# Performance work log

Hardware: AMD Instinct MI355X
Metric: run time of the kernel (lower is better)

The kernel has to match this reference:

```python
import jax, jax.numpy as jnp
import numpy as np

SHAPES = [(76, 76), (38, 38), (19, 19), (1, 20)]  # 3 feature levels + task-token pseudo-level
D, HEADS, NLVL, NPTS = 256, 8, 4, 4
DH = D // HEADS
NLAYERS = 6
B = 2
S = sum(h * w for h, w in SHAPES)  # 7601


def _ref_points():
    # valid_ratios == 1 (no padding) -> normalized pixel-center grid per level, concatenated. [S,2] (x,y)
    refs = []
    for H, W in SHAPES:
        ry, rx = jnp.meshgrid(jnp.linspace(0.5, H - 0.5, H) / H,
                              jnp.linspace(0.5, W - 0.5, W) / W, indexing='ij')
        refs.append(jnp.stack([rx.ravel(), ry.ravel()], -1))
    return jnp.concatenate(refs, 0)


def _layer_norm(x, g, b):
    m = x.mean(-1, keepdims=True)
    v = ((x - m) ** 2).mean(-1, keepdims=True)
    return (x - m) * jax.lax.rsqrt(v + 1e-5) * g + b


def _bilinear(val_l, locx, locy, H, W):
    # val_l: [B, H*W, HEADS, DH]; locx/locy: [B,Q,HEADS,P] normalized coords.
    # grid_sample semantics: align_corners=False, zero padding.
    v = val_l.transpose(0, 2, 1, 3)  # [B,Hh,HW,DH]
    x = locx * W - 0.5
    y = locy * H - 0.5
    x0 = jnp.floor(x)
    y0 = jnp.floor(y)
    wx1 = x - x0
    wy1 = y - y0

    def corner(xi, yi, w):
        valid = ((xi >= 0) & (xi <= W - 1) & (yi >= 0) & (yi <= H - 1)).astype(v.dtype)
        idx = (jnp.clip(yi, 0, H - 1) * W + jnp.clip(xi, 0, W - 1)).astype(jnp.int32)
        idx_t = idx.transpose(0, 2, 1, 3)  # [B,Hh,Q,P]
        Bq, Hh, Q, P = idx_t.shape
        g = jnp.take_along_axis(v, idx_t.reshape(Bq, Hh, Q * P)[..., None], axis=2)
        g = g.reshape(Bq, Hh, Q, P, DH)
        return g * (w * valid).transpose(0, 2, 1, 3)[..., None]

    return (corner(x0, y0, (1 - wx1) * (1 - wy1)) + corner(x0 + 1, y0, wx1 * (1 - wy1))
            + corner(x0, y0 + 1, (1 - wx1) * wy1) + corner(x0 + 1, y0 + 1, wx1 * wy1))


def _msdeform(q, x, ref, Woff, boff, Wa, ba, Wv, bv, Wo, bo):
    Bq, Sq, _ = x.shape
    value = (x @ Wv + bv).reshape(Bq, Sq, HEADS, DH)
    off = (q @ Woff + boff).reshape(Bq, Sq, HEADS, NLVL, NPTS, 2)
    attn = jax.nn.softmax((q @ Wa + ba).reshape(Bq, Sq, HEADS, NLVL * NPTS), -1)
    attn = attn.reshape(Bq, Sq, HEADS, NLVL, NPTS)
    acc = jnp.zeros((Bq, HEADS, Sq, DH), x.dtype)
    start = 0
    for l, (H, W) in enumerate(SHAPES):
        n = H * W
        loc = ref[None, :, None, None, :] + off[:, :, :, l] / jnp.asarray([W, H], x.dtype)
        samp = _bilinear(value[:, start:start + n], loc[..., 0], loc[..., 1], H, W)  # [B,Hh,S,P,DH]
        a = attn[:, :, :, l].transpose(0, 2, 1, 3)  # [B,Hh,S,P]
        acc = acc + (samp * a[..., None]).sum(3)
        start += n
    return acc.transpose(0, 2, 1, 3).reshape(Bq, Sq, D) @ Wo + bo


def reference(src0, src1, src2, pos0, pos1, pos2, task_encoding, task_pos_enc, level_embed,
              W_off, b_off, W_attn, b_attn, W_val, b_val, W_out, b_out,
              W1, b1, W2, b2, g1, beta1, g2, beta2):
    srcs, poss = [src0, src1, src2], [pos0, pos1, pos2]
    sf, pf = [], []
    for l in range(3):
        Bq, C, H, W = srcs[l].shape
        sf.append(srcs[l].reshape(Bq, C, H * W).transpose(0, 2, 1))
        pf.append(poss[l].reshape(Bq, C, H * W).transpose(0, 2, 1) + level_embed[l])
    sf.append(task_encoding)
    pf.append(jnp.broadcast_to(task_pos_enc[None], task_encoding.shape))
    x = jnp.concatenate(sf, 1)   # [B,S,D]
    pos = jnp.concatenate(pf, 1)
    ref = _ref_points()
    for i in range(NLAYERS):
        q = x + pos
        x = _layer_norm(x + _msdeform(q, x, ref, W_off[i], b_off[i], W_attn[i], b_attn[i],
                                      W_val[i], b_val[i], W_out[i], b_out[i]), g1[i], beta1[i])
        x = _layer_norm(x + jax.nn.relu(x @ W1[i] + b1[i]) @ W2[i] + b2[i], g2[i], beta2[i])
    return x


def setup_inputs() -> dict:
    key = jax.random.key(0)
    ks = jax.random.split(key, 20)
    d = {}
    for i, (H, W) in enumerate(SHAPES[:3]):
        d[f'src{i}'] = jax.random.normal(ks[i], (B, D, H, W), jnp.float32)
        d[f'pos{i}'] = jax.random.normal(ks[3 + i], (B, D, H, W), jnp.float32) * 0.1
    d['task_encoding'] = jax.random.normal(ks[6], (B, 20, D), jnp.float32)
    d['task_pos_enc'] = jax.random.normal(ks[7], (20, D), jnp.float32) * 0.1
    d['level_embed'] = jax.random.normal(ks[8], (NLVL, D), jnp.float32) * 0.1

    def w(k, shape, s=0.02):
        return jax.random.normal(k, shape, jnp.float32) * s

    d['W_off'] = w(ks[9], (NLAYERS, D, HEADS * NLVL * NPTS * 2), 0.01)
    d['b_off'] = w(ks[10], (NLAYERS, HEADS * NLVL * NPTS * 2), 0.2)
    d['W_attn'] = w(ks[11], (NLAYERS, D, HEADS * NLVL * NPTS))
    d['b_attn'] = jnp.zeros((NLAYERS, HEADS * NLVL * NPTS), jnp.float32)
    d['W_val'] = w(ks[12], (NLAYERS, D, D))
    d['b_val'] = jnp.zeros((NLAYERS, D), jnp.float32)
    d['W_out'] = w(ks[13], (NLAYERS, D, D))
    d['b_out'] = jnp.zeros((NLAYERS, D), jnp.float32)
    d['W1'] = w(ks[14], (NLAYERS, D, 2048))
    d['b1'] = jnp.zeros((NLAYERS, 2048), jnp.float32)
    d['W2'] = w(ks[15], (NLAYERS, 2048, D))
    d['b2'] = jnp.zeros((NLAYERS, D), jnp.float32)
    d['g1'] = jnp.ones((NLAYERS, D), jnp.float32)
    d['beta1'] = jnp.zeros((NLAYERS, D), jnp.float32)
    d['g2'] = jnp.ones((NLAYERS, D), jnp.float32)
    d['beta2'] = jnp.zeros((NLAYERS, D), jnp.float32)
    return d
```

## Files before the change

kernel.cpp:

```cpp
#include <hip/hip_runtime.h>

#define S_TOT 7601
#define BATCH 2
#define BM (BATCH * S_TOT)
#define DMODEL 256

typedef unsigned short bf16;
typedef __attribute__((ext_vector_type(8))) short v8s;
typedef __attribute__((ext_vector_type(4))) float v4f;

__device__ __forceinline__ float b2f(bf16 u) {
    union { unsigned int i; float f; } v;
    v.i = ((unsigned int)u) << 16;
    return v.f;
}
__device__ __forceinline__ bf16 f2b(float f) {
    union { unsigned int i; float f; } v;
    v.f = f;
    unsigned int r = v.i + 0x7FFFu + ((v.i >> 16) & 1u);
    return (bf16)(r >> 16);
}
__device__ __forceinline__ float ldin(const void* p, size_t i, int isf32) {
    return isf32 ? ((const float*)p)[i] : b2f(((const bf16*)p)[i]);
}

#define GLDS16(gp, lp)                                                          \
    __builtin_amdgcn_global_load_lds(                                           \
        (const __attribute__((address_space(1))) unsigned int*)(gp),            \
        (__attribute__((address_space(3))) unsigned int*)(lp), 16, 0, 0)

__device__ __forceinline__ void xcd_remap(int& bx, int& by) {
    int gx = gridDim.x, gy = gridDim.y;
    int nwg = gx * gy;
    int lin = blockIdx.y * gx + blockIdx.x;
    int q = nwg >> 3, r = nwg & 7;
    int xcd = lin & 7, idx = lin >> 3;
    int lin2 = (xcd < r ? xcd * (q + 1) : r * (q + 1) + (xcd - r) * q) + idx;
    bx = lin2 % gx;
    by = lin2 / gx;
}

__global__ void detect_dtype(const unsigned short* __restrict__ src, int* __restrict__ flag) {
    __shared__ int cnt;
    if (threadIdx.x == 0) cnt = 0;
    __syncthreads();
    int local = 0;
    for (int i = threadIdx.x; i < 16384; i += 256) {
        unsigned int e = (src[i] >> 7) & 0xFFu;
        if (e >= 143u) local++;
    }
    atomicAdd(&cnt, local);
    __syncthreads();
    if (threadIdx.x == 0) *flag = (cnt > 200) ? 1 : 0;
}

__global__ void __launch_bounds__(256) pack_level(const void* __restrict__ src,
                                                  const void* __restrict__ pin,
                                                  const void* __restrict__ lemb, int lrow,
                                                  float* __restrict__ x,
                                                  bf16* __restrict__ pout,
                                                  int HW, int start,
                                                  const int* __restrict__ flag) {
    int isf32 = *flag;
    int i = blockIdx.x * 256 + threadIdx.x;
    int total = BATCH * HW * 256;
    if (i >= total) return;
    int c = i & 255;
    int t = i >> 8;
    int s = t % HW;
    int b = t / HW;
    size_t src_idx = ((size_t)b * 256 + c) * HW + s;
    float sv = ldin(src, src_idx, isf32);
    float pv = ldin(pin, src_idx, isf32) + ldin(lemb, (size_t)lrow * 256 + c, isf32);
    size_t o = ((size_t)b * S_TOT + start + s) * 256 + c;
    x[o] = sv;
    pout[o] = f2b(pv);
}

__global__ void __launch_bounds__(256) pack_task(const void* __restrict__ te,
                                                 const void* __restrict__ tpe,
                                                 float* __restrict__ x,
                                                 bf16* __restrict__ pout,
                                                 const int* __restrict__ flag) {
    int isf32 = *flag;
    int i = blockIdx.x * 256 + threadIdx.x;
    int total = BATCH * 20 * 256;
    if (i >= total) return;
    int c = i & 255;
    int t = (i >> 8) % 20;
    int b = (i >> 8) / 20;
    size_t o = ((size_t)b * S_TOT + 7581 + t) * 256 + c;
    x[o] = ldin(te, ((size_t)b * 20 + t) * 256 + c, isf32);
    pout[o] = f2b(ldin(tpe, (size_t)t * 256 + c, isf32));
}

__global__ void __launch_bounds__(256) make_ref(float* __restrict__ ref) {
    int s = blockIdx.x * 256 + threadIdx.x;
    if (s >= S_TOT) return;
    int H, W, st;
    if (s < 5776)      { H = 76; W = 76; st = 0; }
    else if (s < 7220) { H = 38; W = 38; st = 5776; }
    else if (s < 7581) { H = 19; W = 19; st = 7220; }
    else               { H = 1;  W = 20; st = 7581; }
    int r = s - st;
    int i = r / W, j = r % W;
    ref[s * 2 + 0] = (j + 0.5f) / (float)W;
    ref[s * 2 + 1] = (i + 0.5f) / (float)H;
}

__global__ void __launch_bounds__(256) cast_out(const float* __restrict__ x,
                                                void* __restrict__ o, int n,
                                                const int* __restrict__ flag) {
    int isf32 = *flag;
    int i = blockIdx.x * 256 + threadIdx.x;
    if (i >= n) return;
    if (isf32) ((float*)o)[i] = x[i];
    else       ((bf16*)o)[i] = f2b(x[i]);
}

__global__ void __launch_bounds__(256) cvt_xq(const float* __restrict__ x,
                                              const bf16* __restrict__ pos,
                                              bf16* __restrict__ xb,
                                              bf16* __restrict__ qb, int n4) {
    int i = blockIdx.x * 256 + threadIdx.x;
    if (i >= n4) return;
    float4 xv = ((const float4*)x)[i];
    ushort4 pv = ((const ushort4*)pos)[i];
    ushort4 xo, qo;
    xo.x = f2b(xv.x); xo.y = f2b(xv.y); xo.z = f2b(xv.z); xo.w = f2b(xv.w);
    qo.x = f2b(xv.x + b2f(pv.x));
    qo.y = f2b(xv.y + b2f(pv.y));
    qo.z = f2b(xv.z + b2f(pv.z));
    qo.w = f2b(xv.w + b2f(pv.w));
    ((ushort4*)xb)[i] = xo;
    ((ushort4*)qb)[i] = qo;
}

__global__ void __launch_bounds__(256) transpose_all(const void* __restrict__ Wv,
                                                     const void* __restrict__ Woff,
                                                     const void* __restrict__ Wa,
                                                     const void* __restrict__ Wo,
                                                     const void* __restrict__ W1,
                                                     const void* __restrict__ W2,
                                                     bf16* __restrict__ Wvt,
                                                     bf16* __restrict__ Wqt,
                                                     bf16* __restrict__ Wot,
                                                     bf16* __restrict__ W1t,
                                                     bf16* __restrict__ W2t,
                                                     int L0, const int* __restrict__ flag) {
    int isf32 = *flag;
    int L = (L0 >= 0) ? L0 : (int)blockIdx.y;
    size_t dl = (L0 >= 0) ? 0 : (size_t)blockIdx.y;
    int t = blockIdx.x;
    const void* src; bf16* dst; int K, N; size_t woff; int rowoff = 0;
    if (t < 64)        { src = Wv;   dst = Wvt + dl * 65536;  K = 256;  N = 256;  woff = (size_t)L * 65536; }
    else if (t < 128)  { src = Woff; dst = Wqt + dl * 98304;  K = 256;  N = 256;  woff = (size_t)L * 65536;  t -= 64; }
    else if (t < 160)  { src = Wa;   dst = Wqt + dl * 98304;  K = 256;  N = 128;  woff = (size_t)L * 32768;  rowoff = 256; t -= 128; }
    else if (t < 224)  { src = Wo;   dst = Wot + dl * 65536;  K = 256;  N = 256;  woff = (size_t)L * 65536;  t -= 160; }
    else if (t < 736)  { src = W1;   dst = W1t + dl * 524288; K = 256;  N = 2048; woff = (size_t)L * 524288; t -= 224; }
    else               { src = W2;   dst = W2t + dl * 524288; K = 2048; N = 256;  woff = (size_t)L * 524288; t -= 736; }
    int ntx = N >> 5;
    int tk = (t / ntx) * 32;
    int tn = (t % ntx) * 32;
    __shared__ float tl[32][33];
    int r = threadIdx.x >> 3;
    int c4 = (threadIdx.x & 7) * 4;
#pragma unroll
    for (int i = 0; i < 4; ++i)
        tl[r][c4 + i] = ldin(src, woff + (size_t)(tk + r) * N + tn + c4 + i, isf32);
    __syncthreads();
#pragma unroll
    for (int i = 0; i < 4; ++i)
        dst[(size_t)(tn + r + rowoff) * K + tk + c4 + i] = f2b(tl[c4 + i][r]);
}

__global__ void __launch_bounds__(256) mfma_gemm(const bf16* __restrict__ A,
                                                 const bf16* __restrict__ Wt,
                                                 const void* __restrict__ bias, size_t boff,
                                                 bf16* __restrict__ C,
                                                 int M, int N, int K, int relu,
                                                 const int* __restrict__ flag) {
    int isf32 = *flag;
    __shared__ __align__(16) char smem[32768];
    bf16* As = (bf16*)smem;
    bf16* Bs = (bf16*)smem + 8192;
    int tid = threadIdx.x;
    int lane = tid & 63, wave = tid >> 6;
    int wm = (wave & 1) << 6, wn = (wave >> 1) << 6;
    int bx, by;
    xcd_remap(bx, by);
    int bm = by * 128, bn = bx * 128;
    int q = lane >> 4, l15 = lane & 15;

    v4f acc[4][4];
#pragma unroll
    for (int i = 0; i < 4; ++i)
#pragma unroll
        for (int j = 0; j < 4; ++j) acc[i][j] = (v4f){0.f, 0.f, 0.f, 0.f};

    int r0 = tid >> 2, r1 = r0 + 64;
    int oct = (tid & 3) * 8;
    int am0 = bm + r0; if (am0 >= M) am0 = M - 1;
    int am1 = bm + r1; if (am1 >= M) am1 = M - 1;
    const bf16* ag0 = A + (size_t)am0 * K + oct;
    const bf16* ag1 = A + (size_t)am1 * K + oct;
    const bf16* bg0 = Wt + (size_t)(bn + r0) * K + oct;
    const bf16* bg1 = Wt + (size_t)(bn + r1) * K + oct;
    bf16* lA0 = As + tid * 8;
    bf16* lA1 = As + (tid + 256) * 8;
    bf16* lA2 = As + 4096 + tid * 8;
    bf16* lA3 = As + 4096 + (tid + 256) * 8;
    bf16* lB0 = Bs + tid * 8;
    bf16* lB1 = Bs + (tid + 256) * 8;
    bf16* lB2 = Bs + 4096 + tid * 8;
    bf16* lB3 = Bs + 4096 + (tid + 256) * 8;

    for (int k0 = 0; k0 < K; k0 += 64) {
        GLDS16(ag0 + k0, lA0);
        GLDS16(ag1 + k0, lA1);
        GLDS16(ag0 + k0 + 32, lA2);
        GLDS16(ag1 + k0 + 32, lA3);
        GLDS16(bg0 + k0, lB0);
        GLDS16(bg1 + k0, lB1);
        GLDS16(bg0 + k0 + 32, lB2);
        GLDS16(bg1 + k0 + 32, lB3);
        __syncthreads();
#pragma unroll
        for (int h = 0; h < 2; ++h) {
            v8s a_frag[4], b_frag[4];
#pragma unroll
            for (int mi = 0; mi < 4; ++mi)
                a_frag[mi] = *(const v8s*)&As[h * 4096 + (wm + mi * 16 + l15) * 32 + q * 8];
#pragma unroll
            for (int ni = 0; ni < 4; ++ni)
                b_frag[ni] = *(const v8s*)&Bs[h * 4096 + (wn + ni * 16 + l15) * 32 + q * 8];
#pragma unroll
            for (int mi = 0; mi < 4; ++mi)
#pragma unroll
                for (int ni = 0; ni < 4; ++ni)
                    acc[mi][ni] = __builtin_amdgcn_mfma_f32_16x16x32_bf16(
                        a_frag[mi], b_frag[ni], acc[mi][ni], 0, 0, 0);
        }
        __syncthreads();
    }

    float bcol[4];
#pragma unroll
    for (int ni = 0; ni < 4; ++ni)
        bcol[ni] = ldin(bias, boff + bn + wn + ni * 16 + l15, isf32);
#pragma unroll
    for (int mi = 0; mi < 4; ++mi) {
        int growb = bm + wm + mi * 16 + q * 4;
#pragma unroll
        for (int r = 0; r < 4; ++r) {
            int gm = growb + r;
            if (gm < M) {
                bf16* rowp = C + (size_t)gm * N + bn + wn + l15;
#pragma unroll
                for (int ni = 0; ni < 4; ++ni) {
                    float v = acc[mi][ni][r] + bcol[ni];
                    if (relu) v = fmaxf(v, 0.f);
                    rowp[ni * 16] = f2b(v);
                }
            }
        }
    }
}

__global__ void __launch_bounds__(256) mfma_gemm64(const bf16* __restrict__ A,
                                                   const bf16* __restrict__ Wt,
                                                   const void* __restrict__ bias, size_t boff,
                                                   bf16* __restrict__ C,
                                                   int M, int N, int K, int relu,
                                                   const int* __restrict__ flag) {
    int isf32 = *flag;
    __shared__ __align__(16) char smem[16384];
    bf16* As = (bf16*)smem;
    bf16* Bs = (bf16*)smem + 4096;
    bf16* Cs = (bf16*)smem;
    int tid = threadIdx.x;
    int lane = tid & 63, wave = tid >> 6;
    int wm = (wave & 1) * 32, wn = (wave >> 1) * 32;
    int bx, by;
    xcd_remap(bx, by);
    int bm = by * 64, bn = bx * 64;
    int q = lane >> 4, l15 = lane & 15;

    v4f acc[2][2];
#pragma unroll
    for (int i = 0; i < 2; ++i)
#pragma unroll
        for (int j = 0; j < 2; ++j) acc[i][j] = (v4f){0.f, 0.f, 0.f, 0.f};

    int srow = tid >> 2;
    int oct = (tid & 3) * 8;
    int am = bm + srow; if (am >= M) am = M - 1;
    const bf16* arow = A + (size_t)am * K + oct;
    const bf16* brow = Wt + (size_t)(bn + srow) * K + oct;
    bf16* lA0 = As + tid * 8;
    bf16* lA1 = As + 2048 + tid * 8;
    bf16* lB0 = Bs + tid * 8;
    bf16* lB1 = Bs + 2048 + tid * 8;

    for (int k0 = 0; k0 < K; k0 += 64) {
        GLDS16(arow + k0, lA0);
        GLDS16(arow + k0 + 32, lA1);
        GLDS16(brow + k0, lB0);
        GLDS16(brow + k0 + 32, lB1);
        __syncthreads();
#pragma unroll
        for (int h = 0; h < 2; ++h) {
            v8s a_frag[2], b_frag[2];
#pragma unroll
            for (int mi = 0; mi < 2; ++mi)
                a_frag[mi] = *(const v8s*)&As[h * 2048 + (wm + mi * 16 + l15) * 32 + q * 8];
#pragma unroll
            for (int ni = 0; ni < 2; ++ni)
                b_frag[ni] = *(const v8s*)&Bs[h * 2048 + (wn + ni * 16 + l15) * 32 + q * 8];
#pragma unroll
            for (int mi = 0; mi < 2; ++mi)
#pragma unroll
                for (int ni = 0; ni < 2; ++ni)
                    acc[mi][ni] = __builtin_amdgcn_mfma_f32_16x16x32_bf16(
                        a_frag[mi], b_frag[ni], acc[mi][ni], 0, 0, 0);
        }
        __syncthreads();
    }

#pragma unroll
    for (int ni = 0; ni < 2; ++ni) {
        int cn = wn + ni * 16 + l15;
        float bv = ldin(bias, boff + bn + cn, isf32);
#pragma unroll
        for (int mi = 0; mi < 2; ++mi) {
#pragma unroll
            for (int r = 0; r < 4; ++r) {
                float v = acc[mi][ni][r] + bv;
                if (relu) v = fmaxf(v, 0.f);
                Cs[(wm + mi * 16 + q * 4 + r) * 72 + cn] = f2b(v);
            }
        }
    }
    __syncthreads();
    {
        int row = tid >> 2, seg = tid & 3;
        int gm = bm + row;
        if (gm < M) {
            const bf16* srcp = Cs + row * 72 + seg * 16;
            bf16* dstp = C + (size_t)gm * N + bn + seg * 16;
            *(uint4*)(dstp) = *(const uint4*)(srcp);
            *(uint4*)(dstp + 8) = *(const uint4*)(srcp + 8);
        }
    }
}

__global__ void __launch_bounds__(256) mfma_gemm64k(const bf16* __restrict__ A,
                                                    const bf16* __restrict__ Wt,
                                                    const void* __restrict__ bias, size_t boff,
                                                    bf16* __restrict__ C,
                                                    int M, int N, int K, int relu,
                                                    const int* __restrict__ flag) {
    int isf32 = *flag;
    __shared__ __align__(16) char smem[32768];
    bf16* As = (bf16*)smem;
    bf16* Bs = (bf16*)smem + 8192;
    bf16* Cs = (bf16*)smem;
    int tid = threadIdx.x;
    int lane = tid & 63, wave = tid >> 6;
    int wm = (wave & 1) * 32, wn = (wave >> 1) * 32;
    int bx, by;
    xcd_remap(bx, by);
    int bm = by * 64, bn = bx * 64;
    int q = lane >> 4, l15 = lane & 15;

    v4f acc[2][2];
#pragma unroll
    for (int i = 0; i < 2; ++i)
#pragma unroll
        for (int j = 0; j < 2; ++j) acc[i][j] = (v4f){0.f, 0.f, 0.f, 0.f};

    int srow = tid >> 2;
    int oct = (tid & 3) * 8;
    int am = bm + srow; if (am >= M) am = M - 1;
    const bf16* arow = A + (size_t)am * K + oct;
    const bf16* brow = Wt + (size_t)(bn + srow) * K + oct;

    for (int k0 = 0; k0 < K; k0 += 128) {
#pragma unroll
        for (int h = 0; h < 4; ++h) {
            GLDS16(arow + k0 + h * 32, As + h * 2048 + tid * 8);
            GLDS16(brow + k0 + h * 32, Bs + h * 2048 + tid * 8);
        }
        __syncthreads();
#pragma unroll
        for (int h = 0; h < 4; ++h) {
            v8s a_frag[2], b_frag[2];
#pragma unroll
            for (int mi = 0; mi < 2; ++mi)
                a_frag[mi] = *(const v8s*)&As[h * 2048 + (wm + mi * 16 + l15) * 32 + q * 8];
#pragma unroll
            for (int ni = 0; ni < 2; ++ni)
                b_frag[ni] = *(const v8s*)&Bs[h * 2048 + (wn + ni * 16 + l15) * 32 + q * 8];
#pragma unroll
            for (int mi = 0; mi < 2; ++mi)
#pragma unroll
                for (int ni = 0; ni < 2; ++ni)
                    acc[mi][ni] = __builtin_amdgcn_mfma_f32_16x16x32_bf16(
                        a_frag[mi], b_frag[ni], acc[mi][ni], 0, 0, 0);
        }
        __syncthreads();
    }

#pragma unroll
    for (int ni = 0; ni < 2; ++ni) {
        int cn = wn + ni * 16 + l15;
        float bv = ldin(bias, boff + bn + cn, isf32);
#pragma unroll
        for (int mi = 0; mi < 2; ++mi) {
#pragma unroll
            for (int r = 0; r < 4; ++r) {
                float v = acc[mi][ni][r] + bv;
                if (relu) v = fmaxf(v, 0.f);
                Cs[(wm + mi * 16 + q * 4 + r) * 72 + cn] = f2b(v);
            }
        }
    }
    __syncthreads();
    {
        int row = tid >> 2, seg = tid & 3;
        int gm = bm + row;
        if (gm < M) {
            const bf16* srcp = Cs + row * 72 + seg * 16;
            bf16* dstp = C + (size_t)gm * N + bn + seg * 16;
            *(uint4*)(dstp) = *(const uint4*)(srcp);
            *(uint4*)(dstp + 8) = *(const uint4*)(srcp + 8);
        }
    }
}

__global__ void __launch_bounds__(256) mfma_gemm64_vq(const bf16* __restrict__ xb,
                                                      const bf16* __restrict__ qb,
                                                      const bf16* __restrict__ Wvt,
                                                      const bf16* __restrict__ Wqt,
                                                      const void* __restrict__ bv, size_t obv,
                                                      const void* __restrict__ bo, size_t obo,
                                                      const void* __restrict__ ba, size_t oba,
                                                      bf16* __restrict__ valueo,
                                                      bf16* __restrict__ offo,
                                                      bf16* __restrict__ attno,
                                                      int M, const int* __restrict__ flag) {
    const int K = 256;
    int isf32 = *flag;
    __shared__ __align__(16) char smem[16384];
    bf16* As = (bf16*)smem;
    bf16* Bs = (bf16*)smem + 4096;
    bf16* Cs = (bf16*)smem;
    int tid = threadIdx.x;
    int lane = tid & 63, wave = tid >> 6;
    int wm = (wave & 1) * 32, wn = (wave >> 1) * 32;
    int bx, by;
    xcd_remap(bx, by);
    int bm = by * 64;
    int isV = (bx < 4);
    int bn = isV ? bx * 64 : (bx - 4) * 64;
    const bf16* A = isV ? xb : qb;
    const bf16* Wt = isV ? Wvt : Wqt;
    int q = lane >> 4, l15 = lane & 15;

    v4f acc[2][2];
#pragma unroll
    for (int i = 0; i < 2; ++i)
#pragma unroll
        for (int j = 0; j < 2; ++j) acc[i][j] = (v4f){0.f, 0.f, 0.f, 0.f};

    int srow = tid >> 2;
    int oct = (tid & 3) * 8;
    int am = bm + srow; if (am >= M) am = M - 1;
    const bf16* arow = A + (size_t)am * K + oct;
    const bf16* brow = Wt + (size_t)(bn + srow) * K + oct;
    bf16* lA0 = As + tid * 8;
    bf16* lA1 = As + 2048 + tid * 8;
    bf16* lB0 = Bs + tid * 8;
    bf16* lB1 = Bs + 2048 + tid * 8;

    for (int k0 = 0; k0 < K; k0 += 64) {
        GLDS16(arow + k0, lA0);
        GLDS16(arow + k0 + 32, lA1);
        GLDS16(brow + k0, lB0);
        GLDS16(brow + k0 + 32, lB1);
        __syncthreads();
#pragma unroll
        for (int h = 0; h < 2; ++h) {
            v8s a_frag[2], b_frag[2];
#pragma unroll
            for (int mi = 0; mi < 2; ++mi)
                a_frag[mi] = *(const v8s*)&As[h * 2048 + (wm + mi * 16 + l15) * 32 + q * 8];
#pragma unroll
            for (int ni = 0; ni < 2; ++ni)
                b_frag[ni] = *(const v8s*)&Bs[h * 2048 + (wn + ni * 16 + l15) * 32 + q * 8];
#pragma unroll
            for (int mi = 0; mi < 2; ++mi)
#pragma unroll
                for (int ni = 0; ni < 2; ++ni)
                    acc[mi][ni] = __builtin_amdgcn_mfma_f32_16x16x32_bf16(
                        a_frag[mi], b_frag[ni], acc[mi][ni], 0, 0, 0);
        }
        __syncthreads();
    }

    bf16* outp; int outN, colbase; const void* bptr; size_t bofs;
    if (isV)             { outp = valueo; outN = 256; colbase = bn;       bptr = bv; bofs = obv; }
    else if (bn < 256)   { outp = offo;   outN = 256; colbase = bn;       bptr = bo; bofs = obo; }
    else                 { outp = attno;  outN = 128; colbase = bn - 256; bptr = ba; bofs = oba; }

#pragma unroll
    for (int ni = 0; ni < 2; ++ni) {
        int cn = wn + ni * 16 + l15;
        float bvf = ldin(bptr, bofs + colbase + cn, isf32);
#pragma unroll
        for (int mi = 0; mi < 2; ++mi) {
#pragma unroll
            for (int r = 0; r < 4; ++r) {
                Cs[(wm + mi * 16 + q * 4 + r) * 72 + cn] = f2b(acc[mi][ni][r] + bvf);
            }
        }
    }
    __syncthreads();
    {
        int row = tid >> 2, seg = tid & 3;
        int gm = bm + row;
        if (gm < M) {
            const bf16* srcp = Cs + row * 72 + seg * 16;
            bf16* dstp = outp + (size_t)gm * outN + colbase + seg * 16;
            *(uint4*)(dstp) = *(const uint4*)(srcp);
            *(uint4*)(dstp + 8) = *(const uint4*)(srcp + 8);
        }
    }
}

template<typename TA, int ADDPOS, int RELU>
__global__ void __launch_bounds__(256) gemm_bias(const TA* __restrict__ A,
                                                 const bf16* __restrict__ Apos,
                                                 const void* __restrict__ W, size_t woff,
                                                 const void* __restrict__ bias, size_t boff,
                                                 bf16* __restrict__ C,
                                                 int M, int N, int K,
                                                 const int* __restrict__ flag) {
    int isf32 = *flag;
    __shared__ float As[16][65];
    __shared__ float Bs[16][65];
    int tid = threadIdx.x;
    int tx = tid & 15;
    int ty = tid >> 4;
    int bm = blockIdx.y * 64;
    int bn = blockIdx.x * 64;
    float acc[4][4] = {};
    for (int k0 = 0; k0 < K; k0 += 16) {
#pragma unroll
        for (int e = 0; e < 4; ++e) {
            int idx = tid + e * 256;
            int mm = idx >> 4;
            int kk = idx & 15;
            int gm = bm + mm;
            float av = 0.f;
            if (gm < M) {
                size_t ai = (size_t)gm * K + k0 + kk;
                if (sizeof(TA) == 4) av = ((const float*)A)[ai];
                else                 av = b2f(((const bf16*)A)[ai]);
                if (ADDPOS) av += b2f(Apos[ai]);
            }
            As[kk][mm] = av;
        }
#pragma unroll
        for (int e = 0; e < 4; ++e) {
            int idx = tid + e * 256;
            int kk = idx >> 6;
            int nn = idx & 63;
            int gn = bn + nn;
            Bs[kk][nn] = (gn < N) ? ldin(W, woff + (size_t)(k0 + kk) * N + gn, isf32) : 0.f;
        }
        __syncthreads();
#pragma unroll
        for (int kk = 0; kk < 16; ++kk) {
            float a[4], b[4];
#pragma unroll
            for (int i = 0; i < 4; ++i) a[i] = As[kk][ty + 16 * i];
#pragma unroll
            for (int j = 0; j < 4; ++j) b[j] = Bs[kk][tx + 16 * j];
#pragma unroll
            for (int i = 0; i < 4; ++i)
#pragma unroll
                for (int j = 0; j < 4; ++j) acc[i][j] += a[i] * b[j];
        }
        __syncthreads();
    }
#pragma unroll
    for (int i = 0; i < 4; ++i) {
        int gm = bm + ty + 16 * i;
        if (gm >= M) continue;
#pragma unroll
        for (int j = 0; j < 4; ++j) {
            int gn = bn + tx + 16 * j;
            if (gn >= N) continue;
            float v = acc[i][j] + ldin(bias, boff + gn, isf32);
            if (RELU) v = fmaxf(v, 0.f);
            C[(size_t)gm * N + gn] = f2b(v);
        }
    }
}

__global__ void __launch_bounds__(256) msdeform_sample4(const bf16* __restrict__ value,
                                                        const bf16* __restrict__ off,
                                                        const bf16* __restrict__ logits,
                                                        const float* __restrict__ refpts,
                                                        bf16* __restrict__ out) {
    __shared__ float sAttn[4 * 128];
    __shared__ int2 sIW[4 * 520];
    const int LH[4] = {76, 38, 19, 1};
    const int LW[4] = {76, 38, 19, 20};
    const int LS[4] = {0, 5776, 7220, 7581};
    int tid = threadIdx.x;
    int m0 = blockIdx.x * 4;

    for (int i = tid; i < 4 * 128; i += 256) {
        int r = i >> 7, li = i & 127;
        int m = m0 + r;
        int mc = (m < BM) ? m : BM - 1;
        sAttn[i] = b2f(logits[(size_t)mc * 128 + li]);
    }
    __syncthreads();
    {
        int g = tid >> 3, j = tid & 7;
        float* gp = sAttn + g * 16;
        float e0 = gp[j * 2], e1 = gp[j * 2 + 1];
        float mx = fmaxf(e0, e1);
#pragma unroll
        for (int o = 1; o < 8; o <<= 1) mx = fmaxf(mx, __shfl_xor(mx, o));
        e0 = __expf(e0 - mx);
        e1 = __expf(e1 - mx);
        float sm = e0 + e1;
#pragma unroll
        for (int o = 1; o < 8; o <<= 1) sm += __shfl_xor(sm, o);
        float inv = 1.f / sm;
        gp[j * 2] = e0 * inv;
        gp[j * 2 + 1] = e1 * inv;
    }
    __syncthreads();
    for (int i = tid; i < 4 * 128; i += 256) {
        int r = i >> 7, oi = i & 127;
        int m = m0 + r;
        int mc = (m < BM) ? m : BM - 1;
        int b = mc / S_TOT;
        int s = mc - b * S_TOT;
        int h = oi >> 4;
        int l = (oi >> 2) & 3;
        int H = LH[l], W = LW[l], st = LS[l];
        float fW = (float)W, fH = (float)H;
        float refx = refpts[s * 2 + 0];
        float refy = refpts[s * 2 + 1];
        ushort2 ov = *(const ushort2*)(off + (size_t)mc * 256 + oi * 2);
        float a = sAttn[r * 128 + oi];
        float xpix = (refx + b2f(ov.x) / fW) * fW - 0.5f;
        float ypix = (refy + b2f(ov.y) / fH) * fH - 0.5f;
        float x0f = floorf(xpix), y0f = floorf(ypix);
        int x0 = (int)x0f, y0 = (int)y0f;
        float wx1 = xpix - x0f, wy1 = ypix - y0f;
        float wx0 = 1.f - wx1, wy0 = 1.f - wy1;
        int vb = b * (S_TOT * 256) + h * 32;
        int base = r * 520 + h * 65 + (oi & 15) * 4;
#pragma unroll
        for (int c = 0; c < 4; ++c) {
            int cx = c & 1, cy = c >> 1;
            int xi = x0 + cx, yi = y0 + cy;
            float w = (cx ? wx1 : wx0) * (cy ? wy1 : wy0) * a;
            bool valid = (xi >= 0) && (xi <= W - 1) && (yi >= 0) && (yi <= H - 1);
            int xic = min(max(xi, 0), W - 1), yic = min(max(yi, 0), H - 1);
            int2 d;
            d.x = vb + (st + yic * W + xic) * 256;
            d.y = __float_as_int(valid ? w : 0.f);
            sIW[base + c] = d;
        }
    }
    __syncthreads();
    int r = tid >> 6, u = tid & 63;
    int h = u >> 3, d4 = (u & 7) * 4;
    int m = m0 + r;
    int cb = r * 520 + h * 65;
    float acc0 = 0.f, acc1 = 0.f, acc2 = 0.f, acc3 = 0.f;
#pragma unroll 8
    for (int c = 0; c < 64; ++c) {
        int2 p = sIW[cb + c];
        float w = __int_as_float(p.y);
        ushort4 v = *(const ushort4*)(value + p.x + d4);
        acc0 += w * b2f(v.x);
        acc1 += w * b2f(v.y);
        acc2 += w * b2f(v.z);
        acc3 += w * b2f(v.w);
    }
    if (m < BM) {
        ushort4 o;
        o.x = f2b(acc0); o.y = f2b(acc1); o.z = f2b(acc2); o.w = f2b(acc3);
        *(ushort4*)(out + (size_t)m * 256 + h * 32 + d4) = o;
    }
}

__global__ void __launch_bounds__(256) residual_ln4(float* __restrict__ x,
                                                    const bf16* __restrict__ y,
                                                    const void* __restrict__ g, size_t goff,
                                                    const void* __restrict__ beta, size_t boff,
                                                    const int* __restrict__ flag,
                                                    bf16* __restrict__ xb,
                                                    const bf16* __restrict__ pos,
                                                    bf16* __restrict__ qb) {
    int isf32 = *flag;
    int tid = threadIdx.x;
    int r = tid >> 6, lane = tid & 63;
    int m = blockIdx.x * 4 + r;
    if (m >= BM) return;
    size_t o = (size_t)m * 256 + lane * 4;
    float4 xv = *(const float4*)(x + o);
    ushort4 yv = *(const ushort4*)(y + o);
    float r0 = xv.x + b2f(yv.x), r1 = xv.y + b2f(yv.y);
    float r2 = xv.z + b2f(yv.z), r3 = xv.w + b2f(yv.w);
    float sum = r0 + r1 + r2 + r3;
#pragma unroll
    for (int ofs = 32; ofs > 0; ofs >>= 1) sum += __shfl_xor(sum, ofs);
    float mean = sum * (1.f / 256.f);
    float d0 = r0 - mean, d1 = r1 - mean, d2 = r2 - mean, d3 = r3 - mean;
    float vv = d0 * d0 + d1 * d1 + d2 * d2 + d3 * d3;
#pragma unroll
    for (int ofs = 32; ofs > 0; ofs >>= 1) vv += __shfl_xor(vv, ofs);
    float rstd = rsqrtf(vv * (1.f / 256.f) + 1e-5f);
    int c = lane * 4;
    float o0 = d0 * rstd * ldin(g, goff + c + 0, isf32) + ldin(beta, boff + c + 0, isf32);
    float o1 = d1 * rstd * ldin(g, goff + c + 1, isf32) + ldin(beta, boff + c + 1, isf32);
    float o2 = d2 * rstd * ldin(g, goff + c + 2, isf32) + ldin(beta, boff + c + 2, isf32);
    float o3 = d3 * rstd * ldin(g, goff + c + 3, isf32) + ldin(beta, boff + c + 3, isf32);
    *(float4*)(x + o) = make_float4(o0, o1, o2, o3);
    if (xb) {
        ushort4 xo;
        xo.x = f2b(o0); xo.y = f2b(o1); xo.z = f2b(o2); xo.w = f2b(o3);
        *(ushort4*)(xb + o) = xo;
    }
    if (qb) {
        ushort4 pv = *(const ushort4*)(pos + o);
        ushort4 qo;
        qo.x = f2b(o0 + b2f(pv.x));
        qo.y = f2b(o1 + b2f(pv.y));
        qo.z = f2b(o2 + b2f(pv.z));
        qo.w = f2b(o3 + b2f(pv.w));
        *(ushort4*)(qb + o) = qo;
    }
}

extern "C" void kernel_launch(void* const* d_in, const int* in_sizes, int n_in,
                              void* d_out, int out_size, void* d_ws, size_t ws_size,
                              hipStream_t stream) {
    (void)in_sizes; (void)n_in; (void)out_size;
    const size_t MS = (size_t)BM * DMODEL;

    char* base = (char*)d_ws;
    int* flag    = (int*)base;    base += 256;
    float* x     = (float*)base;  base += MS * 4;
    bf16* value  = (bf16*)base;   base += MS * 2;
    bf16* attnl  = (bf16*)base;   base += (size_t)BM * 128 * 2;
    bf16* pos    = (bf16*)base;   base += MS * 2;
    bf16* offms  = (bf16*)base;   base += MS * 2;
    bf16* yb     = (bf16*)base;   base += MS * 2;
    size_t base_used = (size_t)(base - (char*)d_ws);

    const size_t SZ_WVT = 65536, SZ_WQT = 98304, SZ_WOT = 65536, SZ_W1T = 524288, SZ_W2T = 524288;
    const size_t WB1 = (SZ_WVT + SZ_WQT + SZ_WOT + SZ_W1T + SZ_W2T) * 2;

    bf16* xb = (bf16*)base;
    size_t needB  = base_used + MS * 2 + WB1 + (size_t)S_TOT * 8 + 1024;
    size_t needAH = ((base_used + MS * 2 + 6 * WB1 + (size_t)S_TOT * 8 + 1024 + 255) & ~(size_t)255)
                  + (size_t)BM * 2048 * 2;
    bool FAST = ws_size >= needB;
    bool W6   = ws_size >= needAH;
    int  nL   = W6 ? 6 : 1;

    bf16 *W1t = nullptr, *W2t = nullptr, *Wvt = nullptr, *Wqt = nullptr, *Wot = nullptr;
    float* ref;
    bf16* hiddenF = nullptr;
    bool FULLH = false;
    if (FAST) {
        char* p = (char*)xb + MS * 2;
        Wvt = (bf16*)p;  p += (size_t)nL * SZ_WVT * 2;
        Wqt = (bf16*)p;  p += (size_t)nL * SZ_WQT * 2;
        Wot = (bf16*)p;  p += (size_t)nL * SZ_WOT * 2;
        W1t = (bf16*)p;  p += (size_t)nL * SZ_W1T * 2;
        W2t = (bf16*)p;  p += (size_t)nL * SZ_W2T * 2;
        ref = (float*)p; p += (size_t)S_TOT * 2 * 4;
        size_t used = (size_t)(p - (char*)d_ws);
        used = (used + 255) & ~(size_t)255;
        if (ws_size >= used + (size_t)BM * 2048 * 2) {
            hiddenF = (bf16*)((char*)d_ws + used);
            FULLH = true;
        }
    } else {
        ref = (float*)base;
    }

    bf16* hidden = FULLH ? hiddenF : value;
    const int CH = FULLH ? BM : 2816;

    detect_dtype<<<1, 256, 0, stream>>>((const unsigned short*)d_in[0], flag);

    {
        int HW0 = 76 * 76, HW1 = 38 * 38, HW2 = 19 * 19;
        int n0 = BATCH * HW0 * 256, n1 = BATCH * HW1 * 256, n2 = BATCH * HW2 * 256;
        pack_level<<<(n0 + 255) / 256, 256, 0, stream>>>(d_in[0], d_in[1], d_in[8], 0, x, pos, HW0, 0, flag);
        pack_level<<<(n1 + 255) / 256, 256, 0, stream>>>(d_in[2], d_in[3], d_in[8], 1, x, pos, HW1, 5776, flag);
        pack_level<<<(n2 + 255) / 256, 256, 0, stream>>>(d_in[4], d_in[5], d_in[8], 2, x, pos, HW2, 7220, flag);
        int nt = BATCH * 20 * 256;
        pack_task<<<(nt + 255) / 256, 256, 0, stream>>>(d_in[6], d_in[7], x, pos, flag);
        make_ref<<<(S_TOT + 255) / 256, 256, 0, stream>>>(ref);
    }

    const int GM64 = (BM + 63) / 64;
    const int GR4 = (BM + 3) / 4;
    const int n4 = (int)(MS / 4);

    if (FAST) {
        cvt_xq<<<(n4 + 255) / 256, 256, 0, stream>>>(x, pos, xb, yb, n4);
        if (W6) {
            transpose_all<<<dim3(1248, 6), 256, 0, stream>>>(d_in[13], d_in[9], d_in[11], d_in[15],
                                                             d_in[17], d_in[19],
                                                             Wvt, Wqt, Wot, W1t, W2t, -1, flag);
        }
    }

    for (int L = 0; L < 6; ++L) {
        size_t oW256 = (size_t)L * 256 * 256, ob256 = (size_t)L * 256;
        size_t oW128 = (size_t)L * 256 * 128, ob128 = (size_t)L * 128;
        size_t oW1   = (size_t)L * 256 * 2048, ob1  = (size_t)L * 2048;
        size_t oW2   = (size_t)L * 2048 * 256;

        if (FAST) {
            bf16* WvtL = Wvt + (W6 ? (size_t)L * SZ_WVT : 0);
            bf16* WqtL = Wqt + (W6 ? (size_t)L * SZ_WQT : 0);
            bf16* WotL = Wot + (W6 ? (size_t)L * SZ_WOT : 0);
            bf16* W1tL = W1t + (W6 ? (size_t)L * SZ_W1T : 0);
            bf16* W2tL = W2t + (W6 ? (size_t)L * SZ_W2T : 0);
            if (!W6) {
                transpose_all<<<dim3(1248, 1), 256, 0, stream>>>(d_in[13], d_in[9], d_in[11], d_in[15],
                                                                 d_in[17], d_in[19],
                                                                 Wvt, Wqt, Wot, W1t, W2t, L, flag);
            }
            bf16* qb = yb;
            mfma_gemm64_vq<<<dim3(10, GM64), 256, 0, stream>>>(xb, qb, WvtL, WqtL,
                                                               d_in[14], ob256, d_in[10], ob256,
                                                               d_in[12], ob128,
                                                               value, offms, attnl, BM, flag);

            msdeform_sample4<<<GR4, 256, 0, stream>>>(value, offms, attnl, ref, offms);

            mfma_gemm64<<<dim3(4, GM64), 256, 0, stream>>>(offms, WotL, d_in[16], ob256, yb, BM, 256, 256, 0, flag);
            residual_ln4<<<GR4, 256, 0, stream>>>(x, yb, d_in[21], ob256, d_in[22], ob256, flag, xb, nullptr, nullptr);

            for (int r0 = 0; r0 < BM; r0 += CH) {
                int mc = BM - r0 < CH ? BM - r0 : CH;
                int gmc128 = (mc + 127) / 128;
                int gmc64 = (mc + 63) / 64;
                mfma_gemm<<<dim3(16, gmc128), 256, 0, stream>>>(xb + (size_t)r0 * 256, W1tL, d_in[18], ob1,
                                                                hidden, mc, 2048, 256, 1, flag);
                mfma_gemm64k<<<dim3(4, gmc64), 256, 0, stream>>>(hidden, W2tL, d_in[20], ob256,
                                                                 yb + (size_t)r0 * 256, mc, 256, 2048, 0, flag);
            }
            residual_ln4<<<GR4, 256, 0, stream>>>(x, yb, d_in[23], ob256, d_in[24], ob256, flag, xb,
                                                  (L < 5) ? pos : nullptr, (L < 5) ? yb : nullptr);
        } else {
            dim3 g256(4, GM64);
            dim3 g128(2, GM64);
            gemm_bias<float, 0, 0><<<g256, 256, 0, stream>>>(x, nullptr, d_in[13], oW256, d_in[14], ob256,
                                                             value, BM, 256, 256, flag);
            gemm_bias<float, 1, 0><<<g256, 256, 0, stream>>>(x, pos, d_in[9], oW256, d_in[10], ob256,
                                                             offms, BM, 256, 256, flag);
            gemm_bias<float, 1, 0><<<g128, 256, 0, stream>>>(x, pos, d_in[11], oW128, d_in[12], ob128,
                                                             attnl, BM, 128, 256, flag);
            msdeform_sample4<<<GR4, 256, 0, stream>>>(value, offms, attnl, ref, offms);
            gemm_bias<bf16, 0, 0><<<g256, 256, 0, stream>>>(offms, nullptr, d_in[15], oW256, d_in[16], ob256,
                                                            yb, BM, 256, 256, flag);
            residual_ln4<<<GR4, 256, 0, stream>>>(x, yb, d_in[21], ob256, d_in[22], ob256, flag, nullptr, nullptr, nullptr);
            for (int r0 = 0; r0 < BM; r0 += CH) {
                int mc = BM - r0 < CH ? BM - r0 : CH;
                dim3 gh(32, (mc + 63) / 64);
                dim3 go(4, (mc + 63) / 64);
                gemm_bias<float, 0, 1><<<gh, 256, 0, stream>>>(x + (size_t)r0 * 256, nullptr, d_in[17], oW1,
                                                               d_in[18], ob1, hidden, mc, 2048, 256, flag);
                gemm_bias<bf16, 0, 0><<<go, 256, 0, stream>>>(hidden, nullptr, d_in[19], oW2, d_in[20], ob256,
                                                              yb + (size_t)r0 * 256, mc, 256, 2048, flag);
            }
            residual_ln4<<<GR4, 256, 0, stream>>>(x, yb, d_in[23], ob256, d_in[24], ob256, flag, nullptr, nullptr, nullptr);
        }
    }

    cast_out<<<((int)MS + 255) / 256, 256, 0, stream>>>(x, d_out, (int)MS, flag);
}
```

Measured before the change: 1.135 ms.

## Use 128x128 tiles for fused value/query GEMM, widen sampling loads, fuse output cast

Replaces the 64x64-tile fused value/offset/attention GEMM with a 128x128-tile version that writes results directly without staging through LDS, giving more reuse per block. The deformable sampling gather now loads 8 bf16 per lane and splits the 64 sample points across two lanes, combining them with a shuffle. The final cast_out kernel is removed and the last layer's LayerNorm writes the output in the requested dtype directly. The larger tile cuts the block count and may lower occupancy.

```diff
diff --git a/kernel.cpp b/kernel.cpp
--- a/kernel.cpp
+++ b/kernel.cpp
@@ -8,6 +8,7 @@
 typedef unsigned short bf16;
 typedef __attribute__((ext_vector_type(8))) short v8s;
 typedef __attribute__((ext_vector_type(4))) float v4f;
+typedef __attribute__((ext_vector_type(8))) unsigned short u16x8;
 
 __device__ __forceinline__ float b2f(bf16 u) {
     union { unsigned int i; float f; } v;
@@ -106,16 +107,6 @@
     int i = r / W, j = r % W;
     ref[s * 2 + 0] = (j + 0.5f) / (float)W;
     ref[s * 2 + 1] = (i + 0.5f) / (float)H;
-}
-
-__global__ void __launch_bounds__(256) cast_out(const float* __restrict__ x,
-                                                void* __restrict__ o, int n,
-                                                const int* __restrict__ flag) {
-    int isf32 = *flag;
-    int i = blockIdx.x * 256 + threadIdx.x;
-    if (i >= n) return;
-    if (isf32) ((float*)o)[i] = x[i];
-    else       ((bf16*)o)[i] = f2b(x[i]);
 }
 
 __global__ void __launch_bounds__(256) cvt_xq(const float* __restrict__ x,
@@ -267,6 +258,111 @@
     }
 }
 
+__global__ void __launch_bounds__(256) mfma_gemm_vq128(const bf16* __restrict__ xb,
+                                                       const bf16* __restrict__ qb,
+                                                       const bf16* __restrict__ Wvt,
+                                                       const bf16* __restrict__ Wqt,
+                                                       const void* __restrict__ bv, size_t obv,
+                                                       const void* __restrict__ bo, size_t obo,
+                                                       const void* __restrict__ ba, size_t oba,
+                                                       bf16* __restrict__ valueo,
+                                                       bf16* __restrict__ offo,
+                                                       bf16* __restrict__ attno,
+                                                       int M, const int* __restrict__ flag) {
+    const int K = 256;
+    int isf32 = *flag;
+    __shared__ __align__(16) char smem[32768];
+    bf16* As = (bf16*)smem;
+    bf16* Bs = (bf16*)smem + 8192;
+    int tid = threadIdx.x;
+    int lane = tid & 63, wave = tid >> 6;
+    int wm = (wave & 1) << 6, wn = (wave >> 1) << 6;
+    int bx, by;
+    xcd_remap(bx, by);
+    int bm = by * 128;
+    int isV = (bx < 2);
+    int bn = isV ? bx * 128 : (bx - 2) * 128;
+    const bf16* A = isV ? xb : qb;
+    const bf16* Wt = isV ? Wvt : Wqt;
+    int q = lane >> 4, l15 = lane & 15;
+
+    v4f acc[4][4];
+#pragma unroll
+    for (int i = 0; i < 4; ++i)
+#pragma unroll
+        for (int j = 0; j < 4; ++j) acc[i][j] = (v4f){0.f, 0.f, 0.f, 0.f};
+
+    int r0 = tid >> 2, r1 = r0 + 64;
+    int oct = (tid & 3) * 8;
+    int am0 = bm + r0; if (am0 >= M) am0 = M - 1;
+    int am1 = bm + r1; if (am1 >= M) am1 = M - 1;
+    const bf16* ag0 = A + (size_t)am0 * K + oct;
+    const bf16* ag1 = A + (size_t)am1 * K + oct;
+    const bf16* bg0 = Wt + (size_t)(bn + r0) * K + oct;
+    const bf16* bg1 = Wt + (size_t)(bn + r1) * K + oct;
+    bf16* lA0 = As + tid * 8;
+    bf16* lA1 = As + (tid + 256) * 8;
+    bf16* lA2 = As + 4096 + tid * 8;
+    bf16* lA3 = As + 4096 + (tid + 256) * 8;
+    bf16* lB0 = Bs + tid * 8;
+    bf16* lB1 = Bs + (tid + 256) * 8;
+    bf16* lB2 = Bs + 4096 + tid * 8;
+    bf16* lB3 = Bs + 4096 + (tid + 256) * 8;
+
+    for (int k0 = 0; k0 < K; k0 += 64) {
+        GLDS16(ag0 + k0, lA0);
+        GLDS16(ag1 + k0, lA1);
+        GLDS16(ag0 + k0 + 32, lA2);
+        GLDS16(ag1 + k0 + 32, lA3);
+        GLDS16(bg0 + k0, lB0);
+        GLDS16(bg1 + k0, lB1);
+        GLDS16(bg0 + k0 + 32, lB2);
+        GLDS16(bg1 + k0 + 32, lB3);
+        __syncthreads();
+#pragma unroll
+        for (int h = 0; h < 2; ++h) {
+            v8s a_frag[4], b_frag[4];
+#pragma unroll
+            for (int mi = 0; mi < 4; ++mi)
+                a_frag[mi] = *(const v8s*)&As[h * 4096 + (wm + mi * 16 + l15) * 32 + q * 8];
+#pragma unroll
+            for (int ni = 0; ni < 4; ++ni)
+                b_frag[ni] = *(const v8s*)&Bs[h * 4096 + (wn + ni * 16 + l15) * 32 + q * 8];
+#pragma unroll
+            for (int mi = 0; mi < 4; ++mi)
+#pragma unroll
+                for (int ni = 0; ni < 4; ++ni)
+                    acc[mi][ni] = __builtin_amdgcn_mfma_f32_16x16x32_bf16(
+                        a_frag[mi], b_frag[ni], acc[mi][ni], 0, 0, 0);
+        }
+        __syncthreads();
+    }
+
+    bf16* outp; int outN, colbase; const void* bptr; size_t bofs;
+    if (isV)             { outp = valueo; outN = 256; colbase = bn;       bptr = bv; bofs = obv; }
+    else if (bn < 256)   { outp = offo;   outN = 256; colbase = bn;       bptr = bo; bofs = obo; }
+    else                 { outp = attno;  outN = 128; colbase = bn - 256; bptr = ba; bofs = oba; }
+
+    float bcol[4];
+#pragma unroll
+    for (int ni = 0; ni < 4; ++ni)
+        bcol[ni] = ldin(bptr, bofs + colbase + wn + ni * 16 + l15, isf32);
+#pragma unroll
+    for (int mi = 0; mi < 4; ++mi) {
+        int growb = bm + wm + mi * 16 + q * 4;
+#pragma unroll
+        for (int r = 0; r < 4; ++r) {
+            int gm = growb + r;
+            if (gm < M) {
+                bf16* rowp = outp + (size_t)gm * outN + colbase + wn + l15;
+#pragma unroll
+                for (int ni = 0; ni < 4; ++ni)
+                    rowp[ni * 16] = f2b(acc[mi][ni][r] + bcol[ni]);
+            }
+        }
+    }
+}
+
 __global__ void __launch_bounds__(256) mfma_gemm64(const bf16* __restrict__ A,
                                                    const bf16* __restrict__ Wt,
                                                    const void* __restrict__ bias, size_t boff,
@@ -432,106 +528,6 @@
         if (gm < M) {
             const bf16* srcp = Cs + row * 72 + seg * 16;
             bf16* dstp = C + (size_t)gm * N + bn + seg * 16;
-            *(uint4*)(dstp) = *(const uint4*)(srcp);
-            *(uint4*)(dstp + 8) = *(const uint4*)(srcp + 8);
-        }
-    }
-}
-
-__global__ void __launch_bounds__(256) mfma_gemm64_vq(const bf16* __restrict__ xb,
-                                                      const bf16* __restrict__ qb,
-                                                      const bf16* __restrict__ Wvt,
-                                                      const bf16* __restrict__ Wqt,
-                                                      const void* __restrict__ bv, size_t obv,
-                                                      const void* __restrict__ bo, size_t obo,
-                                                      const void* __restrict__ ba, size_t oba,
-                                                      bf16* __restrict__ valueo,
-                                                      bf16* __restrict__ offo,
-                                                      bf16* __restrict__ attno,
-                                                      int M, const int* __restrict__ flag) {
-    const int K = 256;
-    int isf32 = *flag;
-    __shared__ __align__(16) char smem[16384];
-    bf16* As = (bf16*)smem;
-    bf16* Bs = (bf16*)smem + 4096;
-    bf16* Cs = (bf16*)smem;
-    int tid = threadIdx.x;
-    int lane = tid & 63, wave = tid >> 6;
-    int wm = (wave & 1) * 32, wn = (wave >> 1) * 32;
-    int bx, by;
-    xcd_remap(bx, by);
-    int bm = by * 64;
-    int isV = (bx < 4);
-    int bn = isV ? bx * 64 : (bx - 4) * 64;
-    const bf16* A = isV ? xb : qb;
-    const bf16* Wt = isV ? Wvt : Wqt;
-    int q = lane >> 4, l15 = lane & 15;
-
-    v4f acc[2][2];
-#pragma unroll
-    for (int i = 0; i < 2; ++i)
-#pragma unroll
-        for (int j = 0; j < 2; ++j) acc[i][j] = (v4f){0.f, 0.f, 0.f, 0.f};
-
-    int srow = tid >> 2;
-    int oct = (tid & 3) * 8;
-    int am = bm + srow; if (am >= M) am = M - 1;
-    const bf16* arow = A + (size_t)am * K + oct;
-    const bf16* brow = Wt + (size_t)(bn + srow) * K + oct;
-    bf16* lA0 = As + tid * 8;
-    bf16* lA1 = As + 2048 + tid * 8;
-    bf16* lB0 = Bs + tid * 8;
-    bf16* lB1 = Bs + 2048 + tid * 8;
-
-    for (int k0 = 0; k0 < K; k0 += 64) {
-        GLDS16(arow + k0, lA0);
-        GLDS16(arow + k0 + 32, lA1);
-        GLDS16(brow + k0, lB0);
-        GLDS16(brow + k0 + 32, lB1);
-        __syncthreads();
-#pragma unroll
-        for (int h = 0; h < 2; ++h) {
-            v8s a_frag[2], b_frag[2];
-#pragma unroll
-            for (int mi = 0; mi < 2; ++mi)
-                a_frag[mi] = *(const v8s*)&As[h * 2048 + (wm + mi * 16 + l15) * 32 + q * 8];
-#pragma unroll
-            for (int ni = 0; ni < 2; ++ni)
-                b_frag[ni] = *(const v8s*)&Bs[h * 2048 + (wn + ni * 16 + l15) * 32 + q * 8];
-#pragma unroll
-            for (int mi = 0; mi < 2; ++mi)
-#pragma unroll
-                for (int ni = 0; ni < 2; ++ni)
-                    acc[mi][ni] = __builtin_amdgcn_mfma_f32_16x16x32_bf16(
-                        a_frag[mi], b_frag[ni], acc[mi][ni], 0, 0, 0);
-        }
-        __syncthreads();
-    }
-
-    bf16* outp; int outN, colbase; const void* bptr; size_t bofs;
-    if (isV)             { outp = valueo; outN = 256; colbase = bn;       bptr = bv; bofs = obv; }
-    else if (bn < 256)   { outp = offo;   outN = 256; colbase = bn;       bptr = bo; bofs = obo; }
-    else                 { outp = attno;  outN = 128; colbase = bn - 256; bptr = ba; bofs = oba; }
-
-#pragma unroll
-    for (int ni = 0; ni < 2; ++ni) {
-        int cn = wn + ni * 16 + l15;
-        float bvf = ldin(bptr, bofs + colbase + cn, isf32);
-#pragma unroll
-        for (int mi = 0; mi < 2; ++mi) {
-#pragma unroll
-            for (int r = 0; r < 4; ++r) {
-                Cs[(wm + mi * 16 + q * 4 + r) * 72 + cn] = f2b(acc[mi][ni][r] + bvf);
-            }
-        }
-    }
-    __syncthreads();
-    {
-        int row = tid >> 2, seg = tid & 3;
-        int gm = bm + row;
-        if (gm < M) {
-            const bf16* srcp = Cs + row * 72 + seg * 16;
-            bf16* dstp = outp + (size_t)gm * outN + colbase + seg * 16;
             *(uint4*)(dstp) = *(const uint4*)(srcp);
             *(uint4*)(dstp + 8) = *(const uint4*)(srcp + 8);
         }
@@ -683,24 +679,25 @@
     }
     __syncthreads();
     int r = tid >> 6, u = tid & 63;
-    int h = u >> 3, d4 = (u & 7) * 4;
+    int h = u >> 3, chalf = (u >> 2) & 1, d8 = (u & 3) * 8;
     int m = m0 + r;
-    int cb = r * 520 + h * 65;
-    float acc0 = 0.f, acc1 = 0.f, acc2 = 0.f, acc3 = 0.f;
+    int cb = r * 520 + h * 65 + chalf * 32;
+    float acc[8] = {0.f, 0.f, 0.f, 0.f, 0.f, 0.f, 0.f, 0.f};
 #pragma unroll 8
-    for (int c = 0; c < 64; ++c) {
+    for (int c = 0; c < 32; ++c) {
         int2 p = sIW[cb + c];
         float w = __int_as_float(p.y);
-        ushort4 v = *(const ushort4*)(value + p.x + d4);
-        acc0 += w * b2f(v.x);
-        acc1 += w * b2f(v.y);
-        acc2 += w * b2f(v.z);
-        acc3 += w * b2f(v.w);
-    }
-    if (m < BM) {
-        ushort4 o;
-        o.x = f2b(acc0); o.y = f2b(acc1); o.z = f2b(acc2); o.w = f2b(acc3);
-        *(ushort4*)(out + (size_t)m * 256 + h * 32 + d4) = o;
+        u16x8 v = *(const u16x8*)(value + p.x + d8);
+#pragma unroll
+        for (int k = 0; k < 8; ++k) acc[k] += w * b2f(v[k]);
+    }
+#pragma unroll
+    for (int k = 0; k < 8; ++k) acc[k] += __shfl_xor(acc[k], 4);
+    if (m < BM && chalf == 0) {
+        u16x8 o;
+#pragma unroll
+        for (int k = 0; k < 8; ++k) o[k] = f2b(acc[k]);
+        *(u16x8*)(out + (size_t)m * 256 + h * 32 + d8) = o;
     }
 }
 
@@ -711,7 +708,8 @@
                                                     const int* __restrict__ flag,
                                                     bf16* __restrict__ xb,
                                                     const bf16* __restrict__ pos,
-                                                    bf16* __restrict__ qb) {
+                                                    bf16* __restrict__ qb,
+                                                    void* __restrict__ fout) {
     int isf32 = *flag;
     int tid = threadIdx.x;
     int r = tid >> 6, lane = tid & 63;
@@ -736,6 +734,16 @@
     float o1 = d1 * rstd * ldin(g, goff + c + 1, isf32) + ldin(beta, boff + c + 1, isf32);
     float o2 = d2 * rstd * ldin(g, goff + c + 2, isf32) + ldin(beta, boff + c + 2, isf32);
     float o3 = d3 * rstd * ldin(g, goff + c + 3, isf32) + ldin(beta, boff + c + 3, isf32);
+    if (fout) {
+        if (isf32) {
+            *(float4*)((float*)fout + o) = make_float4(o0, o1, o2, o3);
+        } else {
+            ushort4 fo;
+            fo.x = f2b(o0); fo.y = f2b(o1); fo.z = f2b(o2); fo.w = f2b(o3);
+            *(ushort4*)((bf16*)fout + o) = fo;
+        }
+        return;
+    }
     *(float4*)(x + o) = make_float4(o0, o1, o2, o3);
     if (xb) {
         ushort4 xo;
@@ -819,6 +827,7 @@
     }
 
     const int GM64 = (BM + 63) / 64;
+    const int GM128 = (BM + 127) / 128;
     const int GR4 = (BM + 3) / 4;
     const int n4 = (int)(MS / 4);
 
@@ -836,6 +845,7 @@
         size_t oW128 = (size_t)L * 256 * 128, ob128 = (size_t)L * 128;
         size_t oW1   = (size_t)L * 256 * 2048, ob1  = (size_t)L * 2048;
         size_t oW2   = (size_t)L * 2048 * 256;
+        bool last = (L == 5);
 
         if (FAST) {
             bf16* WvtL = Wvt + (W6 ? (size_t)L * SZ_WVT : 0);
@@ -849,15 +859,16 @@
                                                                  Wvt, Wqt, Wot, W1t, W2t, L, flag);
             }
             bf16* qb = yb;
-            mfma_gemm64_vq<<<dim3(10, GM64), 256, 0, stream>>>(xb, qb, WvtL, WqtL,
-                                                               d_in[14], ob256, d_in[10], ob256,
-                                                               d_in[12], ob128,
-                                                               value, offms, attnl, BM, flag);
+            mfma_gemm_vq128<<<dim3(5, GM128), 256, 0, stream>>>(xb, qb, WvtL, WqtL,
+                                                                d_in[14], ob256, d_in[10], ob256,
+                                                                d_in[12], ob128,
+                                                                value, offms, attnl, BM, flag);
 
             msdeform_sample4<<<GR4, 256, 0, stream>>>(value, offms, attnl, ref, offms);
 
             mfma_gemm64<<<dim3(4, GM64), 256, 0, stream>>>(offms, WotL, d_in[16], ob256, yb, BM, 256, 256, 0, flag);
-            residual_ln4<<<GR4, 256, 0, stream>>>(x, yb, d_in[21], ob256, d_in[22], ob256, flag, xb, nullptr, nullptr);
+            residual_ln4<<<GR4, 256, 0, stream>>>(x, yb, d_in[21], ob256, d_in[22], ob256, flag, xb,
+                                                  nullptr, nullptr, nullptr);
 
             for (int r0 = 0; r0 < BM; r0 += CH) {
                 int mc = BM - r0 < CH ? BM - r0 : CH;
@@ -868,8 +879,11 @@
                 mfma_gemm64k<<<dim3(4, gmc64), 256, 0, stream>>>(hidden, W2tL, d_in[20], ob256,
                                                                  yb + (size_t)r0 * 256, mc, 256, 2048, 0, flag);
             }
-            residual_ln4<<<GR4, 256, 0, stream>>>(x, yb, d_in[23], ob256, d_in[24], ob256, flag, xb,
-                                                  (L < 5) ? pos : nullptr, (L < 5) ? yb : nullptr);
+            residual_ln4<<<GR4, 256, 0, stream>>>(x, yb, d_in[23], ob256, d_in[24], ob256, flag,
+                                                  last ? nullptr : xb,
+                                                  last ? nullptr : pos,
+                                                  last ? nullptr : yb,
+                                                  last ? d_out : nullptr);
         } else {
             dim3 g256(4, GM64);
             dim3 g128(2, GM64);
@@ -882,7 +896,8 @@
             msdeform_sample4<<<GR4, 256, 0, stream>>>(value, offms, attnl, ref, offms);
             gemm_bias<bf16, 0, 0><<<g256, 256, 0, stream>>>(offms, nullptr, d_in[15], oW256, d_in[16], ob256,
                                                             yb, BM, 256, 256, flag);
-            residual_ln4<<<GR4, 256, 0, stream>>>(x, yb, d_in[21], ob256, d_in[22], ob256, flag, nullptr, nullptr, nullptr);
+            residual_ln4<<<GR4, 256, 0, stream>>>(x, yb, d_in[21], ob256, d_in[22], ob256, flag,
+                                                  nullptr, nullptr, nullptr, nullptr);
             for (int r0 = 0; r0 < BM; r0 += CH) {
                 int mc = BM - r0 < CH ? BM - r0 : CH;
                 dim3 gh(32, (mc + 63) / 64);
@@ -892,9 +907,9 @@
                 gemm_bias<bf16, 0, 0><<<go, 256, 0, stream>>>(hidden, nullptr, d_in[19], oW2, d_in[20], ob256,
                                                               yb + (size_t)r0 * 256, mc, 256, 2048, flag);
             }
-            residual_ln4<<<GR4, 256, 0, stream>>>(x, yb, d_in[23], ob256, d_in[24], ob256, flag, nullptr, nullptr, nullptr);
-        }
-    }
-
-    cast_out<<<((int)MS + 255) / 256, 256, 0, stream>>>(x, d_out, (int)MS, flag);
-}
+            residual_ln4<<<GR4, 256, 0, stream>>>(x, yb, d_in[23], ob256, d_in[24], ob256, flag,
+                                                  nullptr, nullptr, nullptr,
+                                                  last ? d_out : nullptr);
+        }
+    }
+}
```

After: 1.097 ms. 3.4% less time.
